# Kernel optimization log

Measured on AMD Instinct MI355X. Metric: run time of the kernel, lower is better.

## Reference

```python
import jax, jax.numpy as jnp
import numpy as np

B, S, NS, MAX_W, H, NH = 4, 512, 8192, 16, 256, 4
DH = H // NH
FF = 4 * H
NEG = -1e9  # finite mask value; fully-padded spans are zeroed at the end anyway


def _layernorm(x, g, b, eps=1e-5):
    m = jnp.mean(x, -1, keepdims=True)
    v = jnp.var(x, -1, keepdims=True)
    return (x - m) * jax.lax.rsqrt(v + eps) * g + b


def _pos_encoding(n, d):
    pos = np.arange(n)[:, None]
    div = np.exp(np.arange(0, d, 2) * (-np.log(10000.0) / d))
    pe = np.zeros((n, d), np.float32)
    pe[:, 0::2] = np.sin(pos * div)
    pe[:, 1::2] = np.cos(pos * div)
    return jnp.asarray(pe)


def setup_inputs():
    key = jax.random.key(0)
    ks = jax.random.split(key, 12)
    sc = 1.0 / np.sqrt(H)
    starts = jax.random.randint(ks[1], (B, NS), 0, S - MAX_W)
    lengths = jax.random.randint(ks[2], (B, NS), 1, MAX_W + 1)
    return {
        "token_reps": jax.random.normal(ks[0], (B, S, H), jnp.float32),
        "span_ids": jnp.stack([starts, starts + lengths], -1),
        "span_masks": jax.random.uniform(ks[3], (B, NS)) < 0.9,
        "pooling": 1,
        "dummy_query": jax.random.normal(ks[4], (H,), jnp.float32) * sc,
        "w_q": jax.random.normal(ks[5], (H, H), jnp.float32) * sc,
        "w_k": jax.random.normal(ks[6], (H, H), jnp.float32) * sc,
        "w_v": jax.random.normal(ks[7], (H, H), jnp.float32) * sc,
        "b_qkv": jnp.zeros((3, H), jnp.float32),
        "w_o": jax.random.normal(ks[8], (H, H), jnp.float32) * sc,
        "b_o": jnp.zeros((H,), jnp.float32),
        "ln_g": jnp.ones((H,), jnp.float32),
        "ln_b": jnp.zeros((H,), jnp.float32),
        "ffn_w1": jax.random.normal(ks[9], (H, FF), jnp.float32) * sc,
        "ffn_b1": jnp.zeros((FF,), jnp.float32),
        "ffn_w2": jax.random.normal(ks[10], (FF, H), jnp.float32) * (1.0 / np.sqrt(FF)),
        "ffn_b2": jnp.zeros((H,), jnp.float32),
    }


def reference(token_reps, span_ids, span_masks, pooling, dummy_query, w_q, w_k, w_v,
              b_qkv, w_o, b_o, ln_g, ln_b, ffn_w1, ffn_b1, ffn_w2, ffn_b2):
    # sequence positional encoding (eval mode -> dropout is identity)
    tr = token_reps + _pos_encoding(S, H)[None]  # [B,S,H]
    # span lengths, zeroed where span is masked out (as in torch code)
    span_len = (span_ids[:, :, 1] - span_ids[:, :, 0]) * span_masks.astype(span_ids.dtype)  # [B,NS]
    offs = jnp.arange(MAX_W)
    valid = offs[None, None, :] < span_len[:, :, None]  # [B,NS,W] True = real token
    pos = jnp.clip(span_ids[:, :, 0:1] + offs[None, None, :], 0, S - 1)  # [B,NS,W]
    # vectorized ragged gather replacing the python double loop
    x = tr[jnp.arange(B)[:, None, None], pos]  # [B,NS,W,H]
    x = jnp.where(valid[..., None], x, 0.0)
    # single-query multi-head cross attention (dummy query attends over span tokens)
    q = (dummy_query @ w_q.T + b_qkv[0]).reshape(NH, DH)
    k = (x @ w_k.T + b_qkv[1]).reshape(B, NS, MAX_W, NH, DH)
    v = (x @ w_v.T + b_qkv[2]).reshape(B, NS, MAX_W, NH, DH)
    logits = jnp.einsum('hd,bnwhd->bnhw', q, k) / np.sqrt(DH)
    logits = jnp.where(valid[:, :, None, :], logits, NEG)
    attn = jax.nn.softmax(logits, axis=-1)
    ctx = jnp.einsum('bnhw,bnwhd->bnhd', attn, v).reshape(B, NS, H)
    out = ctx @ w_o.T + b_o + dummy_query  # residual with the dummy query
    y = _layernorm(out, ln_g, ln_b)
    f = jax.nn.relu(y @ ffn_w1 + ffn_b1) @ ffn_w2 + ffn_b2
    y = _layernorm(f + y, ln_g, ln_b)
    return jnp.where(span_masks[..., None], y, 0.0)  # [B,NS,H]
```

## Files before the change

kernel.cpp:

```cpp
#include <hip/hip_runtime.h>
#include <hip/hip_bf16.h>

#define B_    4
#define S_    512
#define NS_   8192
#define MAXW  16
#define H_    256
#define NH_   4
#define FF_   1024
#define NSPAN (B_*NS_)
#define NEGV  (-1.0e9f)
#define MT    64

typedef short s16x8 __attribute__((ext_vector_type(8)));
typedef float f32x4 __attribute__((ext_vector_type(4)));

__device__ __forceinline__ unsigned short f2bu(float v){
  __hip_bfloat16 h = __float2bfloat16(v);
  union { __hip_bfloat16 h; unsigned short u; } c; c.h = h; return c.u;
}
__device__ __forceinline__ float bu2f(unsigned short u){
  union { unsigned int i; float f; } c; c.i = ((unsigned int)u) << 16; return c.f;
}
__device__ __forceinline__ f32x4 MFMA(s16x8 a, s16x8 b, f32x4 c){
  return __builtin_amdgcn_mfma_f32_16x16x32_bf16(a, b, c, 0, 0, 0);
}

__global__ __launch_bounds__(256) void prep_q_kernel(
    const float* __restrict__ dq, const float* __restrict__ wq,
    const float* __restrict__ wk, const float* __restrict__ bqkv,
    float* __restrict__ qkvec, float* __restrict__ qb)
{
  __shared__ float q_s[H_];
  const int t = threadIdx.x;
  const int h = blockIdx.x;
  float acc = bqkv[t];
  const float4* wr = (const float4*)(wq + (size_t)t*H_);
  #pragma unroll 8
  for (int c = 0; c < 64; ++c) {
    float4 u = wr[c];
    float4 d = *(const float4*)(dq + c*4);
    acc += u.x*d.x + u.y*d.y + u.z*d.z + u.w*d.w;
  }
  q_s[t] = acc;
  __syncthreads();
  float s = 0.f;
  #pragma unroll 8
  for (int d = 0; d < 64; ++d) s += q_s[h*64 + d] * wk[(size_t)(h*64 + d)*H_ + t];
  qkvec[h*H_ + t] = s;
  if (t < 64) {
    float p = q_s[h*64 + t] * bqkv[H_ + h*64 + t];
    #pragma unroll
    for (int off = 32; off; off >>= 1) p += __shfl_down(p, off);
    if (t == 0) qb[h] = p;
  }
}

__global__ __launch_bounds__(256) void prep_all_kernel(
    const float* __restrict__ tok, const float* __restrict__ qkvec,
    const float* __restrict__ qb,
    const float* __restrict__ wv, const float* __restrict__ wo,
    const float* __restrict__ bqkv, const float* __restrict__ bo,
    const float* __restrict__ dq,
    const float* __restrict__ w1, const float* __restrict__ w2,
    float* __restrict__ tr, unsigned short* __restrict__ trbf,
    float* __restrict__ lt, unsigned short* __restrict__ wct,
    unsigned short* __restrict__ w1t, unsigned short* __restrict__ w2t,
    float* __restrict__ zbias)
{
  const int blk = blockIdx.x;
  const int t = threadIdx.x;
  if (blk < 2048) {
    __shared__ float red[4][4];
    const int row = blk;
    const int p = row & (S_ - 1);
    float fac = expf((float)((t >> 1)*2) * (-9.210340371976184f / 256.0f));
    float ang = (float)p * fac;
    float pe = (t & 1) ? cosf(ang) : sinf(ang);
    float v = tok[(size_t)row*H_ + t] + pe;
    tr[(size_t)row*H_ + t] = v;
    trbf[(size_t)row*H_ + t] = f2bu(v);
    float p0 = qkvec[t]*v, p1 = qkvec[H_+t]*v, p2 = qkvec[2*H_+t]*v, p3 = qkvec[3*H_+t]*v;
    const int l = t & 63, wv_ = t >> 6;
    #pragma unroll
    for (int m = 1; m < 64; m <<= 1) {
      p0 += __shfl_xor(p0, m); p1 += __shfl_xor(p1, m);
      p2 += __shfl_xor(p2, m); p3 += __shfl_xor(p3, m);
    }
    if (l == 0) { red[wv_][0]=p0; red[wv_][1]=p1; red[wv_][2]=p2; red[wv_][3]=p3; }
    __syncthreads();
    if (t < 4)
      lt[row*NH_ + t] = (red[0][t]+red[1][t]+red[2][t]+red[3][t] + qb[t]) * 0.125f;
  } else if (blk < 3072) {
    int idx = (blk - 2048)*256 + t;
    int n = idx >> 8, k = idx & 255;
    w1t[idx] = f2bu(w1[(size_t)k*FF_ + n]);
  } else if (blk < 4096) {
    int idx = (blk - 3072)*256 + t;
    int n = idx >> 10, k = idx & 1023;
    w2t[idx] = f2bu(w2[(size_t)k*H_ + n]);
  } else if (blk < 4352) {
    __shared__ float wo_s[H_];
    const int i = blk - 4096;
    wo_s[t] = wo[(size_t)i*H_ + t];
    __syncthreads();
    #pragma unroll
    for (int h = 0; h < NH_; ++h) {
      float s = 0.f;
      #pragma unroll 8
      for (int d = 0; d < 64; ++d)
        s += wo_s[h*64 + d] * wv[(size_t)(h*64 + d)*H_ + t];
      wct[(size_t)i*1024 + h*H_ + t] = f2bu(s);
    }
  } else {
    __shared__ float bv_s[H_];
    bv_s[t] = bqkv[2*H_ + t];
    __syncthreads();
    float acc = bo[t] + dq[t];
    const float4* wr = (const float4*)(wo + (size_t)t*H_);
    #pragma unroll 8
    for (int c = 0; c < 64; ++c) {
      float4 u = wr[c];
      acc += u.x*bv_s[c*4] + u.y*bv_s[c*4+1] + u.z*bv_s[c*4+2] + u.w*bv_s[c*4+3];
    }
    zbias[t] = acc;
  }
}

__global__ __launch_bounds__(256) void pool_kernel(
    const unsigned short* __restrict__ trbf,
    const float* __restrict__ lt,
    const int* __restrict__ span_ids, const int* __restrict__ span_masks,
    int span0, unsigned short* __restrict__ pooled)
{
  const int t = threadIdx.x;
  const int l = t & 63;
  const int wv = t >> 6;
  const int spanL = blockIdx.x * 4 + wv;
  const int span  = span0 + spanL;
  const int b  = span >> 13;
  const int st = span_ids[span*2];
  const int en = span_ids[span*2 + 1];
  const int len = span_masks[span] ? (en - st) : 0;

  const int h = l >> 4, w = l & 15;
  int pos = st + w; pos = pos < 0 ? 0 : (pos > S_-1 ? S_-1 : pos);
  float logit = (w < len) ? lt[(b*S_ + pos)*NH_ + h] : NEGV;
  float mx = logit;
  mx = fmaxf(mx, __shfl_xor(mx, 1));
  mx = fmaxf(mx, __shfl_xor(mx, 2));
  mx = fmaxf(mx, __shfl_xor(mx, 4));
  mx = fmaxf(mx, __shfl_xor(mx, 8));
  float e = expf(logit - mx);
  float se = e;
  se += __shfl_xor(se, 1); se += __shfl_xor(se, 2);
  se += __shfl_xor(se, 4); se += __shfl_xor(se, 8);
  const float av = e / se;

  float acc[NH_][4];
  #pragma unroll
  for (int hh = 0; hh < NH_; ++hh)
    #pragma unroll
    for (int j = 0; j < 4; ++j) acc[hh][j] = 0.f;

  const unsigned short* rb = trbf + (size_t)(b*S_)*H_ + l*4;
  #pragma unroll
  for (int w2 = 0; w2 < MAXW; ++w2) {
    int p2 = st + w2; p2 = p2 < 0 ? 0 : (p2 > S_-1 ? S_-1 : p2);
    ushort4 xv = *(const ushort4*)(rb + (size_t)p2*H_);
    float x0 = bu2f(xv.x), x1 = bu2f(xv.y), x2 = bu2f(xv.z), x3 = bu2f(xv.w);
    #pragma unroll
    for (int hh = 0; hh < NH_; ++hh) {
      float a = __shfl(av, hh*16 + w2);
      acc[hh][0] += a*x0; acc[hh][1] += a*x1;
      acc[hh][2] += a*x2; acc[hh][3] += a*x3;
    }
  }
  unsigned short* pp = pooled + (size_t)spanL * 1024;
  #pragma unroll
  for (int hh = 0; hh < NH_; ++hh) {
    ushort4 o;
    o.x = f2bu(acc[hh][0]); o.y = f2bu(acc[hh][1]);
    o.z = f2bu(acc[hh][2]); o.w = f2bu(acc[hh][3]);
    *(ushort4*)(pp + hh*256 + l*4) = o;
  }
}

__global__ __launch_bounds__(1024, 4) void fused_gemm_kernel(
    const unsigned short* __restrict__ pooled,
    const unsigned short* __restrict__ wct,
    const float* __restrict__ zbias,
    const unsigned short* __restrict__ w1t, const float* __restrict__ b1,
    const unsigned short* __restrict__ w2t, const float* __restrict__ b2,
    const float* __restrict__ lng, const float* __restrict__ lnb,
    const int* __restrict__ masks, int span0,
    float* __restrict__ out)
{
  __shared__ __align__(16) unsigned short bufA[MT*256];
  __shared__ __align__(16) unsigned short bufB[MT*256];
  __shared__ float part_s[MT][16][2];

  const int t = threadIdx.x;
  const int l = t & 63;
  const int w = t >> 6;
  const int ln16 = l & 15;
  const int lg = l >> 4;
  const int sx = ln16 & 7;
  const int m0l = blockIdx.x * MT;
  const int m0g = span0 + m0l;
  const int mycol = w*16 + ln16;

  auto ldA = [&](const unsigned short* base, int row, int slot) -> s16x8 {
    return *(const s16x8*)((const unsigned char*)base + row*512 + ((slot ^ sx) << 4));
  };
  auto sOff = [&](int row, int col) -> int {
    return row*512 + ((((col >> 3) ^ (row & 7))) << 4) + ((col & 7) << 1);
  };

  int srow[2], sslot[2];
  #pragma unroll
  for (int q = 0; q < 2; ++q) { int idx = q*1024 + t; srow[q] = idx >> 5; sslot[q] = idx & 31; }
  const unsigned short* pbase = pooled + (size_t)m0l*1024;

  f32x4 acc[4];
  #pragma unroll
  for (int mf = 0; mf < 4; ++mf) acc[mf] = (f32x4){0,0,0,0};

  const unsigned short* bz = wct + (size_t)mycol*1024 + lg*8;

  unsigned short* As = bufA;
  unsigned short* An = bufB;

  uint4 sr[2];
  #pragma unroll
  for (int q = 0; q < 2; ++q)
    sr[q] = *(const uint4*)(pbase + (size_t)srow[q]*1024 + sslot[q]*8);
  #pragma unroll
  for (int q = 0; q < 2; ++q)
    *(uint4*)((unsigned char*)As + srow[q]*512 + ((sslot[q] ^ (srow[q] & 7)) << 4)) = sr[q];
  __syncthreads();

  s16x8 GA[2], GB[2];
  #define LOADBZ(G, kkg) { G[0] = *(const s16x8*)(bz + (kkg)*64); \
                           G[1] = *(const s16x8*)(bz + (kkg)*64 + 32); }
  LOADBZ(GA, 0); LOADBZ(GB, 1);

  auto zstep = [&](s16x8 (&G)[2], int kk, int kkgnext) {
    #pragma unroll
    for (int half = 0; half < 2; ++half) {
      s16x8 a0 = ldA(As, 0*16 + ln16, kk*8 + half*4 + lg);
      s16x8 a1 = ldA(As, 1*16 + ln16, kk*8 + half*4 + lg);
      s16x8 a2 = ldA(As, 2*16 + ln16, kk*8 + half*4 + lg);
      s16x8 a3 = ldA(As, 3*16 + ln16, kk*8 + half*4 + lg);
      acc[0] = MFMA(a0, G[half], acc[0]); acc[1] = MFMA(a1, G[half], acc[1]);
      acc[2] = MFMA(a2, G[half], acc[2]); acc[3] = MFMA(a3, G[half], acc[3]);
    }
    if (kkgnext < 16) LOADBZ(G, kkgnext);
  };

  #pragma unroll
  for (int c = 0; c < 4; ++c) {
    if (c < 3) {
      #pragma unroll
      for (int q = 0; q < 2; ++q)
        sr[q] = *(const uint4*)(pbase + (size_t)srow[q]*1024 + (c+1)*256 + sslot[q]*8);
    }
    zstep(GA, 0, c*4 + 2);
    zstep(GB, 1, c*4 + 3);
    zstep(GA, 2, c*4 + 4);
    zstep(GB, 3, c*4 + 5);
    if (c < 3) {
      #pragma unroll
      for (int q = 0; q < 2; ++q)
        *(uint4*)((unsigned char*)An + srow[q]*512 + ((sslot[q] ^ (srow[q] & 7)) << 4)) = sr[q];
      __syncthreads();
      unsigned short* tmp = As; As = An; An = tmp;
    }
  }
  #undef LOADBZ

  unsigned short* y_s  = As;
  unsigned short* f1_s = An;
  const float zbv  = zbias[mycol];
  const float g1v  = lng[mycol];
  const float bl1v = lnb[mycol];
  {
    float yv[4][4];
    #pragma unroll
    for (int mf = 0; mf < 4; ++mf)
      #pragma unroll
      for (int r = 0; r < 4; ++r) {
        const int row = mf*16 + lg*4 + r;
        float v = acc[mf][r] + zbv;
        yv[mf][r] = v;
        float s1 = v, s2 = v*v;
        s1 += __shfl_xor(s1,1); s2 += __shfl_xor(s2,1);
        s1 += __shfl_xor(s1,2); s2 += __shfl_xor(s2,2);
        s1 += __shfl_xor(s1,4); s2 += __shfl_xor(s2,4);
        s1 += __shfl_xor(s1,8); s2 += __shfl_xor(s2,8);
        if (ln16 == 0) { part_s[row][w][0] = s1; part_s[row][w][1] = s2; }
      }
    __syncthreads();
    #pragma unroll
    for (int mf = 0; mf < 4; ++mf)
      #pragma unroll
      for (int r = 0; r < 4; ++r) {
        const int row = mf*16 + lg*4 + r;
        float s1 = part_s[row][ln16][0];
        float s2 = part_s[row][ln16][1];
        s1 += __shfl_xor(s1,1); s2 += __shfl_xor(s2,1);
        s1 += __shfl_xor(s1,2); s2 += __shfl_xor(s2,2);
        s1 += __shfl_xor(s1,4); s2 += __shfl_xor(s2,4);
        s1 += __shfl_xor(s1,8); s2 += __shfl_xor(s2,8);
        float mean = s1 * (1.f/H_);
        float var  = s2 * (1.f/H_) - mean*mean; var = fmaxf(var, 0.f);
        float rstd = rsqrtf(var + 1e-5f);
        *(unsigned short*)((unsigned char*)y_s + sOff(row, mycol)) =
            f2bu((yv[mf][r] - mean)*rstd*g1v + bl1v);
      }
  }
  __syncthreads();

  auto gemm8 = [&](const unsigned short* Asrc, const unsigned short* bp, f32x4 (&ac)[4]) {
    s16x8 b0 = *(const s16x8*)bp;
    s16x8 b1 = *(const s16x8*)(bp + 32);
    #pragma unroll
    for (int s = 0; s < 8; ++s) {
      s16x8 bn = b1;
      if (s < 6) bn = *(const s16x8*)(bp + (s+2)*32);
      s16x8 a0 = ldA(Asrc, 0*16 + ln16, s*4 + lg);
      s16x8 a1 = ldA(Asrc, 1*16 + ln16, s*4 + lg);
      s16x8 a2 = ldA(Asrc, 2*16 + ln16, s*4 + lg);
      s16x8 a3 = ldA(Asrc, 3*16 + ln16, s*4 + lg);
      ac[0] = MFMA(a0, b0, ac[0]); ac[1] = MFMA(a1, b0, ac[1]);
      ac[2] = MFMA(a2, b0, ac[2]); ac[3] = MFMA(a3, b0, ac[3]);
      b0 = b1; b1 = bn;
    }
  };

  f32x4 f2acc[4];
  #pragma unroll
  for (int mf = 0; mf < 4; ++mf) f2acc[mf] = (f32x4){0,0,0,0};

  #pragma unroll 1
  for (int nc = 0; nc < 4; ++nc) {
    #pragma unroll
    for (int mf = 0; mf < 4; ++mf) acc[mf] = (f32x4){0,0,0,0};
    gemm8(y_s, w1t + (size_t)(nc*256 + mycol)*256 + lg*8, acc);
    __syncthreads();
    {
      const float bias1 = b1[nc*256 + mycol];
      #pragma unroll
      for (int mf = 0; mf < 4; ++mf)
        #pragma unroll
        for (int r = 0; r < 4; ++r) {
          const int row = mf*16 + lg*4 + r;
          *(unsigned short*)((unsigned char*)f1_s + sOff(row, mycol)) =
              f2bu(fmaxf(acc[mf][r] + bias1, 0.f));
        }
    }
    __syncthreads();
    gemm8(f1_s, w2t + (size_t)mycol*1024 + nc*256 + lg*8, f2acc);
  }

  {
    const float b2v = b2[mycol];
    float vals[4][4];
    #pragma unroll
    for (int mf = 0; mf < 4; ++mf)
      #pragma unroll
      for (int r = 0; r < 4; ++r) {
        const int row = mf*16 + lg*4 + r;
        float resid = bu2f(*(unsigned short*)((unsigned char*)y_s + sOff(row, mycol)));
        float v = f2acc[mf][r] + b2v + resid;
        vals[mf][r] = v;
        float s1 = v, s2 = v*v;
        s1 += __shfl_xor(s1,1); s2 += __shfl_xor(s2,1);
        s1 += __shfl_xor(s1,2); s2 += __shfl_xor(s2,2);
        s1 += __shfl_xor(s1,4); s2 += __shfl_xor(s2,4);
        s1 += __shfl_xor(s1,8); s2 += __shfl_xor(s2,8);
        if (ln16 == 0) { part_s[row][w][0] = s1; part_s[row][w][1] = s2; }
      }
    __syncthreads();
    #pragma unroll
    for (int mf = 0; mf < 4; ++mf)
      #pragma unroll
      for (int r = 0; r < 4; ++r) {
        const int row = mf*16 + lg*4 + r;
        float s1 = part_s[row][ln16][0];
        float s2 = part_s[row][ln16][1];
        s1 += __shfl_xor(s1,1); s2 += __shfl_xor(s2,1);
        s1 += __shfl_xor(s1,2); s2 += __shfl_xor(s2,2);
        s1 += __shfl_xor(s1,4); s2 += __shfl_xor(s2,4);
        s1 += __shfl_xor(s1,8); s2 += __shfl_xor(s2,8);
        float mean = s1 * (1.f/H_);
        float var  = s2 * (1.f/H_) - mean*mean; var = fmaxf(var, 0.f);
        float rstd = rsqrtf(var + 1e-5f);
        const int span = m0g + row;
        int mk = masks[span];
        float o = (vals[mf][r] - mean)*rstd*g1v + bl1v;
        out[(size_t)span*H_ + mycol] = mk ? o : 0.f;
      }
  }
}

extern "C" void kernel_launch(void* const* d_in, const int* in_sizes, int n_in,
                              void* d_out, int out_size, void* d_ws, size_t ws_size,
                              hipStream_t stream) {
  const float* tok      = (const float*)d_in[0];
  const int* span_ids   = (const int*)d_in[1];
  const int* span_masks = (const int*)d_in[2];
  const float* dq   = (const float*)d_in[4];
  const float* wq   = (const float*)d_in[5];
  const float* wk   = (const float*)d_in[6];
  const float* wv   = (const float*)d_in[7];
  const float* bqkv = (const float*)d_in[8];
  const float* wo   = (const float*)d_in[9];
  const float* bo   = (const float*)d_in[10];
  const float* lng  = (const float*)d_in[11];
  const float* lnb  = (const float*)d_in[12];
  const float* w1   = (const float*)d_in[13];
  const float* b1   = (const float*)d_in[14];
  const float* w2   = (const float*)d_in[15];
  const float* b2   = (const float*)d_in[16];

  float* ws    = (float*)d_ws;
  float* tr    = ws;
  float* qkvec = ws + 524288;
  float* qbuf  = qkvec + 1024;
  float* lt    = qbuf + 8;
  float* zbias = lt + 8192;
  unsigned short* ub = (unsigned short*)(zbias + 256);
  unsigned short* trbf   = ub;
  unsigned short* wct    = trbf + 524288;
  unsigned short* w1t    = wct + 262144;
  unsigned short* w2t    = w1t + 262144;
  unsigned short* pooled = w2t + 262144;

  const size_t fixed_bytes = (size_t)(524288 + 1024 + 8 + 8192 + 256)*4
                           + (size_t)(524288 + 262144*3)*2;
  int nb = 1;
  while (nb < 16 && fixed_bytes + (size_t)(NSPAN/nb)*1024*2 > ws_size) nb <<= 1;
  const int spans_b = NSPAN / nb;

  hipLaunchKernelGGL(prep_q_kernel, dim3(NH_), dim3(256), 0, stream,
                     dq, wq, wk, bqkv, qkvec, qbuf);
  hipLaunchKernelGGL(prep_all_kernel, dim3(4353), dim3(256), 0, stream,
                     tok, qkvec, qbuf, wv, wo, bqkv, bo, dq, w1, w2,
                     tr, trbf, lt, wct, w1t, w2t, zbias);

  for (int bi = 0; bi < nb; ++bi) {
    const int span0 = bi * spans_b;
    hipLaunchKernelGGL(pool_kernel, dim3(spans_b/4), dim3(256), 0, stream,
                       trbf, lt, span_ids, span_masks, span0, pooled);
    hipLaunchKernelGGL(fused_gemm_kernel, dim3(spans_b/MT), dim3(1024), 0, stream,
                       pooled, wct, zbias, w1t, b1, w2t, b2,
                       lng, lnb, span_masks, span0, (float*)d_out);
  }
}
```

Baseline: 214.7 us.

## Fuse span pooling into the GEMM kernel and switch to 32x32 MFMA tiles

Span attention pooling now runs inside the GEMM kernel, two heads at a time, writing pooled rows straight into shared memory. This removes the global `pooled` buffer round trip and the separate pool kernel launch. The GEMMs move from 16x16x32 to 32x32x16 bf16 MFMA with 512-thread blocks, and the unused fp32 `tr` write is dropped. In exchange, pooling latency now sits inside the GEMM block, the block shape changes occupancy, and register pressure rises from the 16-wide accumulators.

```diff
diff --git a/kernel.cpp b/kernel.cpp
--- a/kernel.cpp
+++ b/kernel.cpp
@@ -13,7 +13,7 @@
 #define MT    64
 
 typedef short s16x8 __attribute__((ext_vector_type(8)));
-typedef float f32x4 __attribute__((ext_vector_type(4)));
+typedef float f32x16 __attribute__((ext_vector_type(16)));
 
 __device__ __forceinline__ unsigned short f2bu(float v){
   __hip_bfloat16 h = __float2bfloat16(v);
@@ -22,8 +22,8 @@
 __device__ __forceinline__ float bu2f(unsigned short u){
   union { unsigned int i; float f; } c; c.i = ((unsigned int)u) << 16; return c.f;
 }
-__device__ __forceinline__ f32x4 MFMA(s16x8 a, s16x8 b, f32x4 c){
-  return __builtin_amdgcn_mfma_f32_16x16x32_bf16(a, b, c, 0, 0, 0);
+__device__ __forceinline__ f32x16 MFMA32(s16x8 a, s16x8 b, f32x16 c){
+  return __builtin_amdgcn_mfma_f32_32x32x16_bf16(a, b, c, 0, 0, 0);
 }
 
 __global__ __launch_bounds__(256) void prep_q_kernel(
@@ -63,7 +63,7 @@
     const float* __restrict__ bqkv, const float* __restrict__ bo,
     const float* __restrict__ dq,
     const float* __restrict__ w1, const float* __restrict__ w2,
-    float* __restrict__ tr, unsigned short* __restrict__ trbf,
+    unsigned short* __restrict__ trbf,
     float* __restrict__ lt, unsigned short* __restrict__ wct,
     unsigned short* __restrict__ w1t, unsigned short* __restrict__ w2t,
     float* __restrict__ zbias)
@@ -78,7 +78,6 @@
     float ang = (float)p * fac;
     float pe = (t & 1) ? cosf(ang) : sinf(ang);
     float v = tok[(size_t)row*H_ + t] + pe;
-    tr[(size_t)row*H_ + t] = v;
     trbf[(size_t)row*H_ + t] = f2bu(v);
     float p0 = qkvec[t]*v, p1 = qkvec[H_+t]*v, p2 = qkvec[2*H_+t]*v, p3 = qkvec[3*H_+t]*v;
     const int l = t & 63, wv_ = t >> 6;
@@ -127,281 +126,234 @@
   }
 }
 
-__global__ __launch_bounds__(256) void pool_kernel(
-    const unsigned short* __restrict__ trbf,
-    const float* __restrict__ lt,
+__global__ __launch_bounds__(512, 4) void fused_kernel(
+    const unsigned short* __restrict__ trbf, const float* __restrict__ lt,
     const int* __restrict__ span_ids, const int* __restrict__ span_masks,
-    int span0, unsigned short* __restrict__ pooled)
-{
-  const int t = threadIdx.x;
-  const int l = t & 63;
-  const int wv = t >> 6;
-  const int spanL = blockIdx.x * 4 + wv;
-  const int span  = span0 + spanL;
-  const int b  = span >> 13;
-  const int st = span_ids[span*2];
-  const int en = span_ids[span*2 + 1];
-  const int len = span_masks[span] ? (en - st) : 0;
-
-  const int h = l >> 4, w = l & 15;
-  int pos = st + w; pos = pos < 0 ? 0 : (pos > S_-1 ? S_-1 : pos);
-  float logit = (w < len) ? lt[(b*S_ + pos)*NH_ + h] : NEGV;
-  float mx = logit;
-  mx = fmaxf(mx, __shfl_xor(mx, 1));
-  mx = fmaxf(mx, __shfl_xor(mx, 2));
-  mx = fmaxf(mx, __shfl_xor(mx, 4));
-  mx = fmaxf(mx, __shfl_xor(mx, 8));
-  float e = expf(logit - mx);
-  float se = e;
-  se += __shfl_xor(se, 1); se += __shfl_xor(se, 2);
-  se += __shfl_xor(se, 4); se += __shfl_xor(se, 8);
-  const float av = e / se;
-
-  float acc[NH_][4];
-  #pragma unroll
-  for (int hh = 0; hh < NH_; ++hh)
-    #pragma unroll
-    for (int j = 0; j < 4; ++j) acc[hh][j] = 0.f;
-
-  const unsigned short* rb = trbf + (size_t)(b*S_)*H_ + l*4;
-  #pragma unroll
-  for (int w2 = 0; w2 < MAXW; ++w2) {
-    int p2 = st + w2; p2 = p2 < 0 ? 0 : (p2 > S_-1 ? S_-1 : p2);
-    ushort4 xv = *(const ushort4*)(rb + (size_t)p2*H_);
-    float x0 = bu2f(xv.x), x1 = bu2f(xv.y), x2 = bu2f(xv.z), x3 = bu2f(xv.w);
-    #pragma unroll
-    for (int hh = 0; hh < NH_; ++hh) {
-      float a = __shfl(av, hh*16 + w2);
-      acc[hh][0] += a*x0; acc[hh][1] += a*x1;
-      acc[hh][2] += a*x2; acc[hh][3] += a*x3;
-    }
-  }
-  unsigned short* pp = pooled + (size_t)spanL * 1024;
-  #pragma unroll
-  for (int hh = 0; hh < NH_; ++hh) {
-    ushort4 o;
-    o.x = f2bu(acc[hh][0]); o.y = f2bu(acc[hh][1]);
-    o.z = f2bu(acc[hh][2]); o.w = f2bu(acc[hh][3]);
-    *(ushort4*)(pp + hh*256 + l*4) = o;
-  }
-}
-
-__global__ __launch_bounds__(1024, 4) void fused_gemm_kernel(
-    const unsigned short* __restrict__ pooled,
-    const unsigned short* __restrict__ wct,
-    const float* __restrict__ zbias,
+    const unsigned short* __restrict__ wct, const float* __restrict__ zbias,
     const unsigned short* __restrict__ w1t, const float* __restrict__ b1,
     const unsigned short* __restrict__ w2t, const float* __restrict__ b2,
     const float* __restrict__ lng, const float* __restrict__ lnb,
-    const int* __restrict__ masks, int span0,
     float* __restrict__ out)
 {
   __shared__ __align__(16) unsigned short bufA[MT*256];
-  __shared__ __align__(16) unsigned short bufB[MT*256];
-  __shared__ float part_s[MT][16][2];
-
-  const int t = threadIdx.x;
-  const int l = t & 63;
-  const int w = t >> 6;
-  const int ln16 = l & 15;
-  const int lg = l >> 4;
-  const int sx = ln16 & 7;
-  const int m0l = blockIdx.x * MT;
-  const int m0g = span0 + m0l;
-  const int mycol = w*16 + ln16;
-
-  auto ldA = [&](const unsigned short* base, int row, int slot) -> s16x8 {
-    return *(const s16x8*)((const unsigned char*)base + row*512 + ((slot ^ sx) << 4));
+  __shared__ __align__(16) unsigned short bufY[MT*256];
+  __shared__ float attn_s[2][MT][16];
+  __shared__ float part_s[MT][8][2];
+  __shared__ float mv_s[MT][2];
+  __shared__ int meta_rb[MT];
+  __shared__ int meta_len[MT];
+  __shared__ int meta_mk[MT];
+
+  const int t  = threadIdx.x;
+  const int l  = t & 63;
+  const int wv = t >> 6;
+  const int lh = l & 31;
+  const int hs = l >> 5;
+  const int sw = (lh & 7) << 4;
+  const int m0 = blockIdx.x * MT;
+  const int col = wv*32 + lh;
+
+  if (t < MT) {
+    int gs = m0 + t;
+    int st = span_ids[gs*2];
+    int en = span_ids[gs*2 + 1];
+    int mk = span_masks[gs];
+    meta_rb[t]  = (gs >> 13) * S_ + st;
+    meta_len[t] = mk ? (en - st) : 0;
+    meta_mk[t]  = mk;
+  }
+  __syncthreads();
+
+  const f32x16 Z16 = {0,0,0,0,0,0,0,0,0,0,0,0,0,0,0,0};
+
+  auto attn_pass = [&](int p){
+    #pragma unroll
+    for (int q = 0; q < 4; ++q) {
+      int slot = q*512 + t;
+      int w  = slot & 15;
+      int sp = (slot >> 4) & 63;
+      int h2 = slot >> 10;
+      int rb = meta_rb[sp], len = meta_len[sp];
+      float lg_ = (w < len) ? lt[(rb + w)*NH_ + p*2 + h2] : NEGV;
+      float mx = lg_;
+      mx = fmaxf(mx, __shfl_xor(mx,1));
+      mx = fmaxf(mx, __shfl_xor(mx,2));
+      mx = fmaxf(mx, __shfl_xor(mx,4));
+      mx = fmaxf(mx, __shfl_xor(mx,8));
+      float e = expf(lg_ - mx);
+      float se = e;
+      se += __shfl_xor(se,1); se += __shfl_xor(se,2);
+      se += __shfl_xor(se,4); se += __shfl_xor(se,8);
+      attn_s[h2][sp][w] = e / se;
+    }
   };
-  auto sOff = [&](int row, int col) -> int {
-    return row*512 + ((((col >> 3) ^ (row & 7))) << 4) + ((col & 7) << 1);
+
+  auto pool_pass = [&](){
+    #pragma unroll 1
+    for (int i = 0; i < 8; ++i) {
+      int sp = wv*8 + i;
+      int rb = meta_rb[sp];
+      const ushort4* p4 = (const ushort4*)(trbf + (size_t)rb*H_) + l;
+      float a0=0,a1=0,a2=0,a3=0, c0=0,c1=0,c2=0,c3=0;
+      #pragma unroll
+      for (int w2 = 0; w2 < MAXW; ++w2) {
+        ushort4 xv = p4[w2*64];
+        float av0 = attn_s[0][sp][w2];
+        float av1 = attn_s[1][sp][w2];
+        float x0=bu2f(xv.x), x1=bu2f(xv.y), x2=bu2f(xv.z), x3=bu2f(xv.w);
+        a0 += av0*x0; a1 += av0*x1; a2 += av0*x2; a3 += av0*x3;
+        c0 += av1*x0; c1 += av1*x1; c2 += av1*x2; c3 += av1*x3;
+      }
+      int off = sp*512 + ((l*8) ^ ((sp&7)<<4));
+      ushort4 o0, o1;
+      o0.x=f2bu(a0); o0.y=f2bu(a1); o0.z=f2bu(a2); o0.w=f2bu(a3);
+      o1.x=f2bu(c0); o1.y=f2bu(c1); o1.z=f2bu(c2); o1.w=f2bu(c3);
+      *(ushort4*)((char*)bufA + off) = o0;
+      *(ushort4*)((char*)bufY + off) = o1;
+    }
   };
 
-  int srow[2], sslot[2];
+  auto gemm = [&](const unsigned short* buf, const unsigned short* bmat,
+                  int kstride, int kbase, f32x16& ac0, f32x16& ac1){
+    const unsigned short* bp = bmat + (size_t)col*kstride + kbase + hs*8;
+    s16x8 b0 = *(const s16x8*)bp;
+    s16x8 b1 = *(const s16x8*)(bp + 16);
+    s16x8 b2 = *(const s16x8*)(bp + 32);
+    #pragma unroll
+    for (int s = 0; s < 16; ++s) {
+      s16x8 bn = b2;
+      if (s < 13) bn = *(const s16x8*)(bp + (s+3)*16);
+      int cb = (s*32 + hs*16) ^ sw;
+      s16x8 a0 = *(const s16x8*)((const char*)buf + lh*512 + cb);
+      s16x8 a1 = *(const s16x8*)((const char*)buf + (lh+32)*512 + cb);
+      ac0 = MFMA32(a0, b0, ac0);
+      ac1 = MFMA32(a1, b0, ac1);
+      b0 = b1; b1 = b2; b2 = bn;
+    }
+  };
+
+  f32x16 acc0 = Z16, acc1 = Z16;
+  attn_pass(0);
+  __syncthreads();
+  pool_pass();
+  __syncthreads();
+  attn_pass(1);
+  gemm(bufA, wct, 1024, 0,   acc0, acc1);
+  gemm(bufY, wct, 1024, 256, acc0, acc1);
+  __syncthreads();
+  pool_pass();
+  __syncthreads();
+  gemm(bufA, wct, 1024, 512, acc0, acc1);
+  gemm(bufY, wct, 1024, 768, acc0, acc1);
+  __syncthreads();
+
+  const float zbv = zbias[col];
+  const float gv  = lng[col];
+  const float bv  = lnb[col];
   #pragma unroll
-  for (int q = 0; q < 2; ++q) { int idx = q*1024 + t; srow[q] = idx >> 5; sslot[q] = idx & 31; }
-  const unsigned short* pbase = pooled + (size_t)m0l*1024;
-
-  f32x4 acc[4];
+  for (int mf = 0; mf < 2; ++mf)
+    #pragma unroll
+    for (int r = 0; r < 16; ++r) {
+      float v = (mf ? acc1[r] : acc0[r]) + zbv;
+      float s1 = v, s2 = v*v;
+      s1 += __shfl_xor(s1,1);  s2 += __shfl_xor(s2,1);
+      s1 += __shfl_xor(s1,2);  s2 += __shfl_xor(s2,2);
+      s1 += __shfl_xor(s1,4);  s2 += __shfl_xor(s2,4);
+      s1 += __shfl_xor(s1,8);  s2 += __shfl_xor(s2,8);
+      s1 += __shfl_xor(s1,16); s2 += __shfl_xor(s2,16);
+      if (lh == 0) {
+        int row = mf*32 + (r&3) + ((r>>2)<<3) + hs*4;
+        part_s[row][wv][0] = s1; part_s[row][wv][1] = s2;
+      }
+    }
+  __syncthreads();
+  {
+    int row = t >> 3, j = t & 7;
+    float s1 = part_s[row][j][0], s2 = part_s[row][j][1];
+    s1 += __shfl_xor(s1,1); s2 += __shfl_xor(s2,1);
+    s1 += __shfl_xor(s1,2); s2 += __shfl_xor(s2,2);
+    s1 += __shfl_xor(s1,4); s2 += __shfl_xor(s2,4);
+    if (j == 0) {
+      float mean = s1 * (1.f/H_);
+      float var  = s2 * (1.f/H_) - mean*mean; var = fmaxf(var, 0.f);
+      mv_s[row][0] = mean; mv_s[row][1] = rsqrtf(var + 1e-5f);
+    }
+  }
+  __syncthreads();
   #pragma unroll
-  for (int mf = 0; mf < 4; ++mf) acc[mf] = (f32x4){0,0,0,0};
-
-  const unsigned short* bz = wct + (size_t)mycol*1024 + lg*8;
-
-  unsigned short* As = bufA;
-  unsigned short* An = bufB;
-
-  uint4 sr[2];
-  #pragma unroll
-  for (int q = 0; q < 2; ++q)
-    sr[q] = *(const uint4*)(pbase + (size_t)srow[q]*1024 + sslot[q]*8);
-  #pragma unroll
-  for (int q = 0; q < 2; ++q)
-    *(uint4*)((unsigned char*)As + srow[q]*512 + ((sslot[q] ^ (srow[q] & 7)) << 4)) = sr[q];
-  __syncthreads();
-
-  s16x8 GA[2], GB[2];
-  #define LOADBZ(G, kkg) { G[0] = *(const s16x8*)(bz + (kkg)*64); \
-                           G[1] = *(const s16x8*)(bz + (kkg)*64 + 32); }
-  LOADBZ(GA, 0); LOADBZ(GB, 1);
-
-  auto zstep = [&](s16x8 (&G)[2], int kk, int kkgnext) {
-    #pragma unroll
-    for (int half = 0; half < 2; ++half) {
-      s16x8 a0 = ldA(As, 0*16 + ln16, kk*8 + half*4 + lg);
-      s16x8 a1 = ldA(As, 1*16 + ln16, kk*8 + half*4 + lg);
-      s16x8 a2 = ldA(As, 2*16 + ln16, kk*8 + half*4 + lg);
-      s16x8 a3 = ldA(As, 3*16 + ln16, kk*8 + half*4 + lg);
-      acc[0] = MFMA(a0, G[half], acc[0]); acc[1] = MFMA(a1, G[half], acc[1]);
-      acc[2] = MFMA(a2, G[half], acc[2]); acc[3] = MFMA(a3, G[half], acc[3]);
-    }
-    if (kkgnext < 16) LOADBZ(G, kkgnext);
-  };
-
-  #pragma unroll
-  for (int c = 0; c < 4; ++c) {
-    if (c < 3) {
-      #pragma unroll
-      for (int q = 0; q < 2; ++q)
-        sr[q] = *(const uint4*)(pbase + (size_t)srow[q]*1024 + (c+1)*256 + sslot[q]*8);
-    }
-    zstep(GA, 0, c*4 + 2);
-    zstep(GB, 1, c*4 + 3);
-    zstep(GA, 2, c*4 + 4);
-    zstep(GB, 3, c*4 + 5);
-    if (c < 3) {
-      #pragma unroll
-      for (int q = 0; q < 2; ++q)
-        *(uint4*)((unsigned char*)An + srow[q]*512 + ((sslot[q] ^ (srow[q] & 7)) << 4)) = sr[q];
-      __syncthreads();
-      unsigned short* tmp = As; As = An; An = tmp;
-    }
-  }
-  #undef LOADBZ
-
-  unsigned short* y_s  = As;
-  unsigned short* f1_s = An;
-  const float zbv  = zbias[mycol];
-  const float g1v  = lng[mycol];
-  const float bl1v = lnb[mycol];
-  {
-    float yv[4][4];
-    #pragma unroll
-    for (int mf = 0; mf < 4; ++mf)
-      #pragma unroll
-      for (int r = 0; r < 4; ++r) {
-        const int row = mf*16 + lg*4 + r;
-        float v = acc[mf][r] + zbv;
-        yv[mf][r] = v;
-        float s1 = v, s2 = v*v;
-        s1 += __shfl_xor(s1,1); s2 += __shfl_xor(s2,1);
-        s1 += __shfl_xor(s1,2); s2 += __shfl_xor(s2,2);
-        s1 += __shfl_xor(s1,4); s2 += __shfl_xor(s2,4);
-        s1 += __shfl_xor(s1,8); s2 += __shfl_xor(s2,8);
-        if (ln16 == 0) { part_s[row][w][0] = s1; part_s[row][w][1] = s2; }
-      }
-    __syncthreads();
-    #pragma unroll
-    for (int mf = 0; mf < 4; ++mf)
-      #pragma unroll
-      for (int r = 0; r < 4; ++r) {
-        const int row = mf*16 + lg*4 + r;
-        float s1 = part_s[row][ln16][0];
-        float s2 = part_s[row][ln16][1];
-        s1 += __shfl_xor(s1,1); s2 += __shfl_xor(s2,1);
-        s1 += __shfl_xor(s1,2); s2 += __shfl_xor(s2,2);
-        s1 += __shfl_xor(s1,4); s2 += __shfl_xor(s2,4);
-        s1 += __shfl_xor(s1,8); s2 += __shfl_xor(s2,8);
-        float mean = s1 * (1.f/H_);
-        float var  = s2 * (1.f/H_) - mean*mean; var = fmaxf(var, 0.f);
-        float rstd = rsqrtf(var + 1e-5f);
-        *(unsigned short*)((unsigned char*)y_s + sOff(row, mycol)) =
-            f2bu((yv[mf][r] - mean)*rstd*g1v + bl1v);
-      }
-  }
-  __syncthreads();
-
-  auto gemm8 = [&](const unsigned short* Asrc, const unsigned short* bp, f32x4 (&ac)[4]) {
-    s16x8 b0 = *(const s16x8*)bp;
-    s16x8 b1 = *(const s16x8*)(bp + 32);
-    #pragma unroll
-    for (int s = 0; s < 8; ++s) {
-      s16x8 bn = b1;
-      if (s < 6) bn = *(const s16x8*)(bp + (s+2)*32);
-      s16x8 a0 = ldA(Asrc, 0*16 + ln16, s*4 + lg);
-      s16x8 a1 = ldA(Asrc, 1*16 + ln16, s*4 + lg);
-      s16x8 a2 = ldA(Asrc, 2*16 + ln16, s*4 + lg);
-      s16x8 a3 = ldA(Asrc, 3*16 + ln16, s*4 + lg);
-      ac[0] = MFMA(a0, b0, ac[0]); ac[1] = MFMA(a1, b0, ac[1]);
-      ac[2] = MFMA(a2, b0, ac[2]); ac[3] = MFMA(a3, b0, ac[3]);
-      b0 = b1; b1 = bn;
-    }
-  };
-
-  f32x4 f2acc[4];
-  #pragma unroll
-  for (int mf = 0; mf < 4; ++mf) f2acc[mf] = (f32x4){0,0,0,0};
-
+  for (int mf = 0; mf < 2; ++mf)
+    #pragma unroll
+    for (int r = 0; r < 16; ++r) {
+      int row = mf*32 + (r&3) + ((r>>2)<<3) + hs*4;
+      float v = (mf ? acc1[r] : acc0[r]) + zbv;
+      float y = (v - mv_s[row][0]) * mv_s[row][1] * gv + bv;
+      int off = row*512 + ((col*2) ^ ((row&7)<<4));
+      *(unsigned short*)((char*)bufY + off) = f2bu(y);
+    }
+  __syncthreads();
+
+  f32x16 f20 = Z16, f21 = Z16;
   #pragma unroll 1
   for (int nc = 0; nc < 4; ++nc) {
-    #pragma unroll
-    for (int mf = 0; mf < 4; ++mf) acc[mf] = (f32x4){0,0,0,0};
-    gemm8(y_s, w1t + (size_t)(nc*256 + mycol)*256 + lg*8, acc);
-    __syncthreads();
-    {
-      const float bias1 = b1[nc*256 + mycol];
+    f32x16 a0c = Z16, a1c = Z16;
+    gemm(bufY, w1t + (size_t)(nc*256)*256, 256, 0, a0c, a1c);
+    __syncthreads();
+    const float b1v = b1[nc*256 + col];
+    #pragma unroll
+    for (int mf = 0; mf < 2; ++mf)
       #pragma unroll
-      for (int mf = 0; mf < 4; ++mf)
-        #pragma unroll
-        for (int r = 0; r < 4; ++r) {
-          const int row = mf*16 + lg*4 + r;
-          *(unsigned short*)((unsigned char*)f1_s + sOff(row, mycol)) =
-              f2bu(fmaxf(acc[mf][r] + bias1, 0.f));
-        }
-    }
-    __syncthreads();
-    gemm8(f1_s, w2t + (size_t)mycol*1024 + nc*256 + lg*8, f2acc);
-  }
-
+      for (int r = 0; r < 16; ++r) {
+        int row = mf*32 + (r&3) + ((r>>2)<<3) + hs*4;
+        float v = fmaxf((mf ? a1c[r] : a0c[r]) + b1v, 0.f);
+        int off = row*512 + ((col*2) ^ ((row&7)<<4));
+        *(unsigned short*)((char*)bufA + off) = f2bu(v);
+      }
+    __syncthreads();
+    gemm(bufA, w2t, 1024, nc*256, f20, f21);
+  }
+
+  const float b2v = b2[col];
+  #pragma unroll
+  for (int mf = 0; mf < 2; ++mf)
+    #pragma unroll
+    for (int r = 0; r < 16; ++r) {
+      int row = mf*32 + (r&3) + ((r>>2)<<3) + hs*4;
+      int off = row*512 + ((col*2) ^ ((row&7)<<4));
+      float rd = bu2f(*(const unsigned short*)((const char*)bufY + off));
+      float v = (mf ? f21[r] : f20[r]) + b2v + rd;
+      float s1 = v, s2 = v*v;
+      s1 += __shfl_xor(s1,1);  s2 += __shfl_xor(s2,1);
+      s1 += __shfl_xor(s1,2);  s2 += __shfl_xor(s2,2);
+      s1 += __shfl_xor(s1,4);  s2 += __shfl_xor(s2,4);
+      s1 += __shfl_xor(s1,8);  s2 += __shfl_xor(s2,8);
+      s1 += __shfl_xor(s1,16); s2 += __shfl_xor(s2,16);
+      if (lh == 0) { part_s[row][wv][0] = s1; part_s[row][wv][1] = s2; }
+    }
+  __syncthreads();
   {
-    const float b2v = b2[mycol];
-    float vals[4][4];
-    #pragma unroll
-    for (int mf = 0; mf < 4; ++mf)
-      #pragma unroll
-      for (int r = 0; r < 4; ++r) {
-        const int row = mf*16 + lg*4 + r;
-        float resid = bu2f(*(unsigned short*)((unsigned char*)y_s + sOff(row, mycol)));
-        float v = f2acc[mf][r] + b2v + resid;
-        vals[mf][r] = v;
-        float s1 = v, s2 = v*v;
-        s1 += __shfl_xor(s1,1); s2 += __shfl_xor(s2,1);
-        s1 += __shfl_xor(s1,2); s2 += __shfl_xor(s2,2);
-        s1 += __shfl_xor(s1,4); s2 += __shfl_xor(s2,4);
-        s1 += __shfl_xor(s1,8); s2 += __shfl_xor(s2,8);
-        if (ln16 == 0) { part_s[row][w][0] = s1; part_s[row][w][1] = s2; }
-      }
-    __syncthreads();
-    #pragma unroll
-    for (int mf = 0; mf < 4; ++mf)
-      #pragma unroll
-      for (int r = 0; r < 4; ++r) {
-        const int row = mf*16 + lg*4 + r;
-        float s1 = part_s[row][ln16][0];
-        float s2 = part_s[row][ln16][1];
-        s1 += __shfl_xor(s1,1); s2 += __shfl_xor(s2,1);
-        s1 += __shfl_xor(s1,2); s2 += __shfl_xor(s2,2);
-        s1 += __shfl_xor(s1,4); s2 += __shfl_xor(s2,4);
-        s1 += __shfl_xor(s1,8); s2 += __shfl_xor(s2,8);
-        float mean = s1 * (1.f/H_);
-        float var  = s2 * (1.f/H_) - mean*mean; var = fmaxf(var, 0.f);
-        float rstd = rsqrtf(var + 1e-5f);
-        const int span = m0g + row;
-        int mk = masks[span];
-        float o = (vals[mf][r] - mean)*rstd*g1v + bl1v;
-        out[(size_t)span*H_ + mycol] = mk ? o : 0.f;
-      }
-  }
+    int row = t >> 3, j = t & 7;
+    float s1 = part_s[row][j][0], s2 = part_s[row][j][1];
+    s1 += __shfl_xor(s1,1); s2 += __shfl_xor(s2,1);
+    s1 += __shfl_xor(s1,2); s2 += __shfl_xor(s2,2);
+    s1 += __shfl_xor(s1,4); s2 += __shfl_xor(s2,4);
+    if (j == 0) {
+      float mean = s1 * (1.f/H_);
+      float var  = s2 * (1.f/H_) - mean*mean; var = fmaxf(var, 0.f);
+      mv_s[row][0] = mean; mv_s[row][1] = rsqrtf(var + 1e-5f);
+    }
+  }
+  __syncthreads();
+  #pragma unroll
+  for (int mf = 0; mf < 2; ++mf)
+    #pragma unroll
+    for (int r = 0; r < 16; ++r) {
+      int row = mf*32 + (r&3) + ((r>>2)<<3) + hs*4;
+      int off = row*512 + ((col*2) ^ ((row&7)<<4));
+      float rd = bu2f(*(const unsigned short*)((const char*)bufY + off));
+      float v = (mf ? f21[r] : f20[r]) + b2v + rd;
+      float o = (v - mv_s[row][0]) * mv_s[row][1] * gv + bv;
+      out[(size_t)(m0 + row)*H_ + col] = meta_mk[row] ? o : 0.f;
+    }
 }
 
 extern "C" void kernel_launch(void* const* d_in, const int* in_sizes, int n_in,
@@ -425,36 +377,22 @@
   const float* b2   = (const float*)d_in[16];
 
   float* ws    = (float*)d_ws;
-  float* tr    = ws;
-  float* qkvec = ws + 524288;
+  float* qkvec = ws;
   float* qbuf  = qkvec + 1024;
   float* lt    = qbuf + 8;
   float* zbias = lt + 8192;
   unsigned short* ub = (unsigned short*)(zbias + 256);
-  unsigned short* trbf   = ub;
-  unsigned short* wct    = trbf + 524288;
-  unsigned short* w1t    = wct + 262144;
-  unsigned short* w2t    = w1t + 262144;
-  unsigned short* pooled = w2t + 262144;
-
-  const size_t fixed_bytes = (size_t)(524288 + 1024 + 8 + 8192 + 256)*4
-                           + (size_t)(524288 + 262144*3)*2;
-  int nb = 1;
-  while (nb < 16 && fixed_bytes + (size_t)(NSPAN/nb)*1024*2 > ws_size) nb <<= 1;
-  const int spans_b = NSPAN / nb;
+  unsigned short* trbf = ub;
+  unsigned short* wct  = trbf + 524288;
+  unsigned short* w1t  = wct + 262144;
+  unsigned short* w2t  = w1t + 262144;
 
   hipLaunchKernelGGL(prep_q_kernel, dim3(NH_), dim3(256), 0, stream,
                      dq, wq, wk, bqkv, qkvec, qbuf);
   hipLaunchKernelGGL(prep_all_kernel, dim3(4353), dim3(256), 0, stream,
                      tok, qkvec, qbuf, wv, wo, bqkv, bo, dq, w1, w2,
-                     tr, trbf, lt, wct, w1t, w2t, zbias);
-
-  for (int bi = 0; bi < nb; ++bi) {
-    const int span0 = bi * spans_b;
-    hipLaunchKernelGGL(pool_kernel, dim3(spans_b/4), dim3(256), 0, stream,
-                       trbf, lt, span_ids, span_masks, span0, pooled);
-    hipLaunchKernelGGL(fused_gemm_kernel, dim3(spans_b/MT), dim3(1024), 0, stream,
-                       pooled, wct, zbias, w1t, b1, w2t, b2,
-                       lng, lnb, span_masks, span0, (float*)d_out);
-  }
-}
+                     trbf, lt, wct, w1t, w2t, zbias);
+  hipLaunchKernelGGL(fused_kernel, dim3(NSPAN/MT), dim3(512), 0, stream,
+                     trbf, lt, span_ids, span_masks, wct, zbias,
+                     w1t, b1, w2t, b2, lng, lnb, (float*)d_out);
+}
```

Result: slower. 353.9 us (+64.9%).
